# Kernel tuning notes

Hardware: AMD Instinct MI355X
Metric: run time of the kernel (lower is better)

Reference implementation:

```python
import jax, jax.numpy as jnp
import numpy as np

B, DIM, HEADS, WS, H, W = 8, 192, 6, 8, 128, 128
HD = DIM // HEADS


def _make_coords(h, w, ws):
    # matches torch buffers: channel 0 = x (width axis), channel 1 = y (height axis)
    ref_w = jnp.linspace(-1.0, 1.0, w)
    ref_h = jnp.linspace(-1.0, 1.0, h)
    img_ref = jnp.stack(jnp.meshgrid(ref_w, ref_h, indexing='ij'), 0).transpose(0, 2, 1)  # (2,h,w)
    wh, ww = h // ws, w // ws
    win_ref = img_ref.reshape(2, wh, ws, ww, ws).mean(axis=(2, 4)).reshape(2, wh, 1, ww, 1)
    bch = jnp.arange(ws) * 2.0 / (h - 1); bch = bch - bch.mean()
    bcw = jnp.arange(ws) * 2.0 / (w - 1); bcw = bcw - bcw.mean()
    ech = jnp.tile(bch, wh)                      # (wh*ws,)
    ecw = jnp.tile(bcw, ww)                      # (ww*ws,)
    offs = jnp.stack(jnp.meshgrid(ecw, ech, indexing='ij'), 0).transpose(0, 2, 1)  # (2, wh*ws, ww*ws)
    offs = offs.reshape(2, wh, ws, ww, ws)
    return win_ref + offs, offs


def _rel_index(ws):
    ch, cw = np.meshgrid(np.arange(ws), np.arange(ws), indexing='ij')
    cf = np.stack([ch.ravel(), cw.ravel()])           # (2, ws*ws)
    rel = cf[:, :, None] - cf[:, None, :]             # (2, n, n)
    return jnp.asarray((rel[0] + ws - 1) * (2 * ws - 1) + (rel[1] + ws - 1))


def _grid_sample(img, grid):
    # F.grid_sample: bilinear, padding_mode='zeros', align_corners=True
    # img (N,C,H,W), grid (N,Ho,Wo,2) with [..,0]=x, [..,1]=y in [-1,1]
    n, c, h, w = img.shape
    gx = (grid[..., 0] + 1.0) * 0.5 * (w - 1)
    gy = (grid[..., 1] + 1.0) * 0.5 * (h - 1)
    x0 = jnp.floor(gx); y0 = jnp.floor(gy)
    wx1 = gx - x0; wy1 = gy - y0

    def gather(ix, iy, wgt):
        valid = (ix >= 0) & (ix <= w - 1) & (iy >= 0) & (iy <= h - 1)
        ixc = jnp.clip(ix, 0, w - 1).astype(jnp.int32)
        iyc = jnp.clip(iy, 0, h - 1).astype(jnp.int32)
        vals = jax.vmap(lambda im, yy, xx: im[:, yy, xx])(img, iyc, ixc)  # (N,C,Ho,Wo)
        return vals * (wgt * valid)[:, None]

    return (gather(x0, y0, (1 - wx1) * (1 - wy1)) + gather(x0 + 1, y0, wx1 * (1 - wy1))
            + gather(x0, y0 + 1, (1 - wx1) * wy1) + gather(x0 + 1, y0 + 1, wx1 * wy1))


def _forward(x, var, qkv_w, qkv_b, bias_w, bias_b, scale_w, scale_b, proj_w, proj_b, rel_table):
    b, c, h, w = x.shape
    wh, ww = h // WS, w // WS
    n_pred = b * HEADS
    base, offs = _make_coords(h, w, WS)

    topk = int(0.8 * h * w)
    var3 = var.reshape(b, c, h * w)
    _, idx = jax.lax.top_k(var3, topk)
    bi = jnp.arange(b)[:, None, None]; ci = jnp.arange(c)[None, :, None]
    mask = jnp.zeros((b, c, h * w), bool).at[bi, ci, idx].set(True)
    x_var = x * jnp.where(mask, 1.0, 0.6).reshape(b, c, h, w).astype(x.dtype)

    # sampling biases/scales: AvgPool(ws) -> LeakyReLU -> 1x1 conv
    pooled = jax.nn.leaky_relu(x_var.reshape(b, c, wh, WS, ww, WS).mean(axis=(3, 5)))
    biases = (jnp.einsum('bchw,oc->bohw', pooled, bias_w) + bias_b[None, :, None, None])
    biases = biases.reshape(n_pred, 2, wh, ww) / jnp.array([w // WS, h // WS], x.dtype)[None, :, None, None]
    scales = (jnp.einsum('bchw,oc->bohw', pooled, scale_w) + scale_b[None, :, None, None]).reshape(n_pred, 2, wh, ww)

    coords = base[None] + offs[None] * scales[:, :, :, None, :, None] + biases[:, :, :, None, :, None]
    grid = coords.transpose(0, 2, 3, 4, 5, 1).reshape(n_pred, h, w, 2)

    # qkv 1x1 conv, split into per-head maps
    qkv = jnp.einsum('bchw,oc->bohw', x, qkv_w) + qkv_b[None, :, None, None]
    qkv = qkv.reshape(b, 3, HEADS, HD, h, w).transpose(1, 0, 2, 3, 4, 5).reshape(3, n_pred, HD, h, w)
    q, k, v = qkv[0], qkv[1], qkv[2]

    ks = _grid_sample(k, grid)
    vs = _grid_sample(v, grid)

    def to_windows(t):  # (b*heads, hd, h, w) -> (b*wh*ww, heads, ws*ws, hd)
        return t.reshape(b, HEADS, HD, wh, WS, ww, WS).transpose(0, 3, 5, 1, 4, 6, 2).reshape(b * wh * ww, HEADS, WS * WS, HD)

    qw, kw, vw = to_windows(q), to_windows(ks), to_windows(vs)
    scores = jnp.einsum('wnid,wnjd->wnij', qw, kw) * (HD ** -0.5)
    rel_bias = rel_table[_rel_index(WS)].transpose(2, 0, 1)  # (heads, ws*ws, ws*ws)
    attn = jax.nn.softmax(scores + rel_bias[None], axis=-1)
    out = jnp.einsum('wnij,wnjd->wnid', attn, vw)
    out = out.reshape(b, wh, ww, HEADS, WS, WS, HD).transpose(0, 3, 6, 1, 4, 2, 5).reshape(b, c, h, w)
    return jnp.einsum('bchw,oc->bohw', out, proj_w) + proj_b[None, :, None, None]


def setup_inputs() -> dict:
    key = jax.random.key(0)
    ks = jax.random.split(key, 8)
    f = jnp.float32
    return {
        'x': jax.random.normal(ks[0], (B, DIM, H, W), f),
        'var': jax.random.uniform(ks[1], (B, DIM, H, W), f),
        'qkv_w': jax.random.normal(ks[2], (3 * DIM, DIM), f) * 0.05,
        'qkv_b': jnp.zeros((3 * DIM,), f),
        'bias_w': jax.random.normal(ks[3], (2 * HEADS, DIM), f) * 0.05,
        'bias_b': jnp.zeros((2 * HEADS,), f),
        'scale_w': jax.random.normal(ks[4], (2 * HEADS, DIM), f) * 0.05,
        'scale_b': jnp.zeros((2 * HEADS,), f),
        'proj_w': jax.random.normal(ks[5], (DIM, DIM), f) * 0.05,
        'proj_b': jnp.zeros((DIM,), f),
        'rel_table': jax.random.normal(ks[6], ((2 * WS - 1) ** 2, HEADS), f) * 0.02,
    }


def reference(x, var, qkv_w, qkv_b, bias_w, bias_b, scale_w, scale_b, proj_w, proj_b, rel_table):
    return _forward(x, var, qkv_w, qkv_b, bias_w, bias_b, scale_w, scale_b, proj_w, proj_b, rel_table)
```

## Files before the change

kernel.cpp:

```cpp
#include <hip/hip_runtime.h>
#include <hip/hip_bf16.h>
#include <math.h>

constexpr int BB = 8, CCH = 192, IH = 128, IW = 128;
constexpr int WSZ = 8;
constexpr int NWIN = 256;
constexpr int NH = 6, HDIM = 32;
constexpr int NPIX = IH * IW;
constexpr int TOPK = 13107;

typedef __attribute__((ext_vector_type(8))) short bf16x8;
typedef __attribute__((ext_vector_type(4))) float f32x4;
typedef __attribute__((ext_vector_type(4))) unsigned short u16x4;
typedef __attribute__((ext_vector_type(8))) unsigned short u16x8;

__device__ __forceinline__ unsigned short f2bf(float f) {
    __hip_bfloat16 h = __float2bfloat16(f);
    return __builtin_bit_cast(unsigned short, h);
}
__device__ __forceinline__ float bf2f(unsigned short u) {
    return __uint_as_float((unsigned)u << 16);
}
__device__ __forceinline__ unsigned monot(float f) {
    unsigned u = __float_as_uint(f);
    return (u & 0x80000000u) ? ~u : (u | 0x80000000u);
}

__global__ __launch_bounds__(512) void k1_pool(const float* __restrict__ x,
                                               const float* __restrict__ var,
                                               float* __restrict__ pooled) {
    int row = blockIdx.x;
    const float4* vrow4 = (const float4*)(var + (size_t)row * NPIX);
    const float4* xrow4 = (const float4*)(x + (size_t)row * NPIX);
    const float* xrow = x + (size_t)row * NPIX;
    int tid = threadIdx.x;
    int wv = tid >> 6, lane = tid & 63;

    constexpr int CAP = 320;
    __shared__ unsigned histP[2][2048];
    __shared__ unsigned hist256[256];
    __shared__ unsigned wtot[8];
    __shared__ unsigned s_prefix, s_rem, s_cnt, s_thr, s_need;
    __shared__ unsigned candKey[CAP], candIdx[CAP];
    __shared__ unsigned cand_cnt, eq_cnt;
    __shared__ unsigned eq_idx[64];
    __shared__ float pooled_s[256];

    for (int i = tid; i < 2 * 2048; i += 512) ((unsigned*)histP)[i] = 0;
    if (tid < 256) pooled_s[tid] = 0.f;
    if (tid == 0) { cand_cnt = 0; eq_cnt = 0; }
    __syncthreads();

    int hc = lane & 1;
#pragma unroll
    for (int j = 0; j < 8; ++j) {
        float4 v4 = vrow4[tid + 512 * j];
        float vv[4] = {v4.x, v4.y, v4.z, v4.w};
#pragma unroll
        for (int c = 0; c < 4; ++c) {
            unsigned bk = monot(vv[c]) >> 20;
            atomicAdd(&histP[hc][bk >> 1], 1u << ((bk & 1) << 4));
        }
    }
    __syncthreads();

    {
        unsigned h8[8]; unsigned tsum = 0;
#pragma unroll
        for (int w = 0; w < 4; ++w) {
            unsigned w0 = histP[0][tid * 4 + w];
            unsigned w1 = histP[1][tid * 4 + w];
            h8[2 * w]     = (w0 & 0xFFFFu) + (w1 & 0xFFFFu);
            h8[2 * w + 1] = (w0 >> 16) + (w1 >> 16);
            tsum += h8[2 * w] + h8[2 * w + 1];
        }
        unsigned s = tsum;
#pragma unroll
        for (int off = 1; off < 64; off <<= 1) {
            unsigned t = __shfl(s, lane + off);
            if (lane + off < 64) s += t;
        }
        if (lane == 0) wtot[wv] = s;
        __syncthreads();
        unsigned crossTot = 0;
        for (int w = wv + 1; w < 8; ++w) crossTot += wtot[w];
        unsigned above = crossTot + (s - tsum);
        if (above < TOPK && above + tsum >= TOPK) {
            unsigned cum = above;
            for (int i = 7; i >= 0; --i) {
                if (cum < TOPK && cum + h8[i] >= TOPK) {
                    s_prefix = (unsigned)(tid * 8 + i);
                    s_rem = TOPK - cum;
                    s_cnt = h8[i];
                }
                cum += h8[i];
            }
        }
    }
    __syncthreads();

    unsigned prefix = s_prefix, rem2 = s_rem, cnt = s_cnt;
    int prefbits = 12;

    while (cnt > CAP && prefbits < 32) {
        int nb = (32 - prefbits >= 8) ? 8 : (32 - prefbits);
        int nbuck = 1 << nb;
        __syncthreads();
        for (int i = tid; i < nbuck; i += 512) hist256[i] = 0;
        __syncthreads();
        int shift = 32 - prefbits - nb;
#pragma unroll
        for (int j = 0; j < 8; ++j) {
            float4 v4 = vrow4[tid + 512 * j];
            float vv[4] = {v4.x, v4.y, v4.z, v4.w};
#pragma unroll
            for (int c = 0; c < 4; ++c) {
                unsigned mm = monot(vv[c]);
                if ((mm >> (nb + shift)) == prefix)
                    atomicAdd(&hist256[(mm >> shift) & (nbuck - 1)], 1u);
            }
        }
        __syncthreads();
        if (wv == 0) {
            int bpl = nbuck > 64 ? nbuck / 64 : 1;
            int nlanes = nbuck / bpl;
            unsigned hh[4] = {0, 0, 0, 0};
            unsigned lsum = 0;
#pragma unroll
            for (int i = 0; i < 4; ++i) {
                if (i < bpl && lane < nlanes) hh[i] = hist256[lane * bpl + i];
                lsum += hh[i];
            }
            unsigned s = lsum;
#pragma unroll
            for (int off = 1; off < 64; off <<= 1) {
                unsigned t = __shfl(s, lane + off);
                if (lane + off < 64) s += t;
            }
            unsigned above = s - lsum;
            if (lane < nlanes && above < rem2 && above + lsum >= rem2) {
                unsigned cum = above;
                for (int i = bpl - 1; i >= 0; --i) {
                    if (cum < rem2 && cum + hh[i] >= rem2) {
                        s_prefix = (prefix << nb) | (unsigned)(lane * bpl + i);
                        s_rem = rem2 - cum;
                        s_cnt = hh[i];
                    }
                    cum += hh[i];
                }
            }
        }
        __syncthreads();
        prefix = s_prefix; rem2 = s_rem; cnt = s_cnt;
        prefbits += nb;
    }

    int pshift = 32 - prefbits;

#pragma unroll
    for (int j = 0; j < 8; ++j) {
        float4 v4 = vrow4[tid + 512 * j];
        float4 x4 = xrow4[tid + 512 * j];
        float vv[4] = {v4.x, v4.y, v4.z, v4.w};
        float xv[4] = {x4.x, x4.y, x4.z, x4.w};
        float part = 0.f;
#pragma unroll
        for (int c = 0; c < 4; ++c) {
            unsigned mm = monot(vv[c]);
            unsigned g = (pshift == 0) ? mm : (mm >> pshift);
            float mult = (g > prefix) ? 1.0f : 0.6f;
            if (g == prefix) {
                unsigned pos = atomicAdd(&cand_cnt, 1u);
                if (pos < CAP) {
                    candKey[pos] = mm;
                    candIdx[pos] = (unsigned)(4 * tid + 2048 * j + c);
                }
            }
            part += xv[c] * mult;
        }
        part += __shfl_xor(part, 1);
        part += __shfl_xor(part, 32);
        if ((lane & 1) == 0 && lane < 32)
            atomicAdd(&pooled_s[(2 * j + (tid >> 8)) * 16 + ((tid >> 1) & 15)], part);
    }
    __syncthreads();

    int cc = (int)min(cand_cnt, (unsigned)CAP);
    for (int ci = tid; ci < cc; ci += 512) {
        unsigned my = candKey[ci];
        unsigned kgt = 0, keq = 0;
        for (int e = 0; e < cc; ++e) {
            unsigned o = candKey[e];
            kgt += (o > my);
            keq += (o == my);
        }
        if (kgt < rem2 && kgt + keq >= rem2) {
            s_thr = my;
            s_need = rem2 - kgt;
        }
    }
    __syncthreads();
    unsigned thr = s_thr, need_eq = s_need;
    for (int ci = tid; ci < cc; ci += 512)
        if (candKey[ci] == thr) {
            unsigned pos = atomicAdd(&eq_cnt, 1u);
            if (pos < 64) eq_idx[pos] = candIdx[ci];
        }
    __syncthreads();
    int ecnt = (int)min(eq_cnt, 64u);
    if (tid == 0) {
        for (int a = 1; a < ecnt; ++a) {
            unsigned key = eq_idx[a]; int q = a - 1;
            while (q >= 0 && eq_idx[q] > key) { eq_idx[q + 1] = eq_idx[q]; --q; }
            eq_idx[q + 1] = key;
        }
    }
    __syncthreads();

    for (int ci = tid; ci < cc; ci += 512) {
        unsigned key = candKey[ci], idx = candIdx[ci];
        bool inset;
        if (key > thr) inset = true;
        else if (key < thr) inset = false;
        else {
            unsigned rank = 0;
            for (int e = 0; e < ecnt; ++e) rank += (eq_idx[e] < idx);
            inset = (rank < need_eq);
        }
        if (inset) {
            int y = (int)(idx >> 7), xx = (int)(idx & 127);
            atomicAdd(&pooled_s[(y >> 3) * 16 + (xx >> 3)], 0.4f * xrow[idx]);
        }
    }
    __syncthreads();

    if (tid < 256) {
        float s = pooled_s[tid] * (1.0f / 64.0f);
        float pv = s > 0.f ? s : 0.01f * s;
        pooled[(size_t)row * NWIN + tid] = pv;
    }
}

__global__ __launch_bounds__(64) void k2_sb(const float* __restrict__ pooled,
                                            const float* __restrict__ bias_w,
                                            const float* __restrict__ bias_b,
                                            const float* __restrict__ scale_w,
                                            const float* __restrict__ scale_b,
                                            float* __restrict__ sb) {
    int blk = blockIdx.x;
    int b = blk / NWIN, w = blk % NWIN;
    int tid = threadIdx.x;
    __shared__ float pcol[CCH];
    __shared__ float res[24];
    for (int c = tid; c < CCH; c += 64) pcol[c] = pooled[(size_t)(b * CCH + c) * NWIN + w];
    __syncthreads();
    if (tid < 24) {
        bool isScale = tid >= 12;
        int o = isScale ? tid - 12 : tid;
        const float* Wt = isScale ? scale_w : bias_w;
        float acc = 0.f;
        for (int c = 0; c < CCH; ++c) acc += Wt[o * CCH + c] * pcol[c];
        acc += (isScale ? scale_b[o] : bias_b[o]);
        if (!isScale) acc *= (1.0f / 16.0f);
        res[tid] = acc;
    }
    __syncthreads();
    if (tid < NH) {
        int p = b * NH + tid;
        float4 v;
        v.x = res[12 + 2 * tid];
        v.y = res[12 + 2 * tid + 1];
        v.z = res[2 * tid];
        v.w = res[2 * tid + 1];
        ((float4*)sb)[(size_t)p * NWIN + w] = v;
    }
}

__global__ __launch_bounds__(256) void kw_conv(const float* __restrict__ qkv_w,
                                               const float* __restrict__ proj_w,
                                               unsigned short* __restrict__ wbf) {
    int i4 = blockIdx.x * 256 + threadIdx.x;
    float4 v = (i4 < 27648) ? ((const float4*)qkv_w)[i4]
                            : ((const float4*)proj_w)[i4 - 27648];
    u16x4 pk = { f2bf(v.x), f2bf(v.y), f2bf(v.z), f2bf(v.w) };
    ((u16x4*)wbf)[i4] = pk;
}

__global__ __launch_bounds__(256) void k0_xpose(const float* __restrict__ x,
                                                unsigned short* __restrict__ xt) {
    __shared__ unsigned short T[64][200];
    int px0 = blockIdx.x * 64;
    int b = blockIdx.y;
    int tid = threadIdx.x;
    int px = tid & 63, cg = tid >> 6;

#pragma unroll
    for (int j8 = 0; j8 < 6; ++j8) {
        u16x8 pk;
#pragma unroll
        for (int j = 0; j < 8; ++j)
            pk[j] = f2bf(x[(size_t)(b * CCH + cg * 48 + j8 * 8 + j) * NPIX + px0 + px]);
        *(u16x8*)&T[px][cg * 48 + j8 * 8] = pk;
    }
    __syncthreads();
#pragma unroll
    for (int i = 0; i < 6; ++i) {
        int u = tid + 256 * i;
        int p2 = u / 24, cb = u % 24;
        *(u16x8*)&xt[((size_t)(b * NPIX) + px0 + p2) * CCH + cb * 8] = *(const u16x8*)&T[p2][cb * 8];
    }
}

template <bool FAST>
__global__ __launch_bounds__(256) void k3_mfma(const float* __restrict__ x,
                                               const unsigned short* __restrict__ xt,
                                               const unsigned short* __restrict__ wq,
                                               const float* __restrict__ qkv_b,
                                               unsigned short* __restrict__ qb,
                                               unsigned short* __restrict__ kb,
                                               unsigned short* __restrict__ vb) {
    constexpr int BN = 128, KC = 64, KCP = 72;
    __shared__ unsigned short Ws[CCH][KCP];
    __shared__ unsigned short Xt[BN][KCP];
    int px0 = blockIdx.x * BN;
    int t = blockIdx.y, b = blockIdx.z;
    int o0 = t * CCH;
    int tid = threadIdx.x;
    int wv = tid >> 6, lane = tid & 63, lr = lane & 15, lg = lane >> 4;

    f32x4 acc[3][8];
#pragma unroll
    for (int i = 0; i < 3; ++i)
#pragma unroll
        for (int j = 0; j < 8; ++j) acc[i][j] = (f32x4){0.f, 0.f, 0.f, 0.f};

    int spx = tid & 127, skg = tid >> 7;

    for (int k0 = 0; k0 < CCH; k0 += KC) {
#pragma unroll
        for (int i = 0; i < 6; ++i) {
            int u = tid + 256 * i;
            int o = u >> 3, kb8 = u & 7;
            *(u16x8*)&Ws[o][kb8 * 8] = *(const u16x8*)&wq[(size_t)(o0 + o) * CCH + k0 + kb8 * 8];
        }
        if (FAST) {
#pragma unroll
            for (int i = 0; i < 4; ++i) {
                int u = tid + 256 * i;
                int px = u >> 3, kb8 = u & 7;
                *(u16x8*)&Xt[px][kb8 * 8] =
                    *(const u16x8*)&xt[((size_t)(b * NPIX) + px0 + px) * CCH + k0 + kb8 * 8];
            }
        } else {
            const float* xcol = &x[(size_t)(b * CCH + k0 + skg * 32) * NPIX + px0 + spx];
#pragma unroll
            for (int j8 = 0; j8 < 4; ++j8) {
                u16x8 pk;
#pragma unroll
                for (int j = 0; j < 8; ++j) pk[j] = f2bf(xcol[(size_t)(j8 * 8 + j) * NPIX]);
                *(u16x8*)&Xt[spx][skg * 32 + j8 * 8] = pk;
            }
        }
        __syncthreads();
#pragma unroll
        for (int kk = 0; kk < KC; kk += 32) {
            bf16x8 af[3], bfr[8];
#pragma unroll
            for (int i = 0; i < 3; ++i)
                af[i] = *(const bf16x8*)&Ws[wv * 48 + i * 16 + lr][kk + lg * 8];
#pragma unroll
            for (int j = 0; j < 8; ++j)
                bfr[j] = *(const bf16x8*)&Xt[j * 16 + lr][kk + lg * 8];
#pragma unroll
            for (int i = 0; i < 3; ++i)
#pragma unroll
                for (int j = 0; j < 8; ++j)
                    acc[i][j] = __builtin_amdgcn_mfma_f32_16x16x32_bf16(af[i], bfr[j], acc[i][j], 0, 0, 0);
        }
        __syncthreads();
    }

#pragma unroll
    for (int i = 0; i < 3; ++i) {
        int och = wv * 48 + i * 16 + lg * 4;
        float b0 = qkv_b[o0 + och], b1 = qkv_b[o0 + och + 1];
        float b2 = qkv_b[o0 + och + 2], b3 = qkv_b[o0 + och + 3];
#pragma unroll
        for (int j = 0; j < 8; ++j) {
            int px = px0 + lr + j * 16;
            u16x4 pk = { f2bf(acc[i][j][0] + b0), f2bf(acc[i][j][1] + b1),
                         f2bf(acc[i][j][2] + b2), f2bf(acc[i][j][3] + b3) };
            if (t == 0) {
                *(u16x4*)&qb[((size_t)b * NPIX + px) * CCH + och] = pk;
            } else {
                int head = och >> 5, d = och & 31;
                unsigned short* dst = (t == 1) ? kb : vb;
                *(u16x4*)&dst[(((size_t)(b * NH + head)) * NPIX + px) * HDIM + d] = pk;
            }
        }
    }
}

__global__ __launch_bounds__(256) void k4_attn(unsigned short* __restrict__ qatt,
                                               const unsigned short* __restrict__ kb,
                                               const unsigned short* __restrict__ vb,
                                               const float* __restrict__ sb,
                                               const float* __restrict__ rel_table) {
    int tid = threadIdx.x;
    int wv = tid >> 6, lane = tid & 63, lr = lane & 15, lg = lane >> 4;
    int head = blockIdx.y, b = blockIdx.z;
    int win = blockIdx.x * 4 + wv;
    int wy = win >> 4, wx = win & 15;
    int p = b * NH + head;

    __shared__ float rel_s[225];
    __shared__ unsigned short Vl[4][64][33];
    __shared__ unsigned short Pl[4][64][68];

    if (tid < 225) rel_s[tid] = rel_table[tid * NH + head];

    bf16x8 qf[4];
#pragma unroll
    for (int tq = 0; tq < 4; ++tq) {
        int q = tq * 16 + lr;
        int pix = (wy * 8 + (q >> 3)) * IW + wx * 8 + (q & 7);
        qf[tq] = *(const bf16x8*)&qatt[((size_t)b * NPIX + pix) * CCH + head * HDIM + lg * 8];
    }

    float4 sbv = ((const float4*)sb)[(size_t)p * NWIN + win];
    bf16x8 kf[4];
#pragma unroll
    for (int mi = 0; mi < 4; ++mi) {
        int px = mi * 16 + lr;
        int dy = px >> 3, dx = px & 7;
        int yg = wy * 8 + dy, xg = wx * 8 + dx;
        float gx = -1.0f + xg * (2.0f / 127.0f) + ((float)dx - 3.5f) * (2.0f / 127.0f) * sbv.x + sbv.z;
        float gy = -1.0f + yg * (2.0f / 127.0f) + ((float)dy - 3.5f) * (2.0f / 127.0f) * sbv.y + sbv.w;
        float fx = (gx + 1.0f) * 0.5f * 127.0f;
        float fy = (gy + 1.0f) * 0.5f * 127.0f;
        float x0f = floorf(fx), y0f = floorf(fy);
        float wx1 = fx - x0f, wy1 = fy - y0f;
        int ix0 = (int)x0f, iy0 = (int)y0f;
        int ix1 = ix0 + 1, iy1 = iy0 + 1;
        float w00 = (1.0f - wx1) * (1.0f - wy1);
        float w10 = wx1 * (1.0f - wy1);
        float w01 = (1.0f - wx1) * wy1;
        float w11 = wx1 * wy1;
        bool vX0 = (ix0 >= 0) && (ix0 < IW), vX1 = (ix1 >= 0) && (ix1 < IW);
        bool vY0 = (iy0 >= 0) && (iy0 < IH), vY1 = (iy1 >= 0) && (iy1 < IH);
        if (!(vX0 && vY0)) w00 = 0.f;
        if (!(vX1 && vY0)) w10 = 0.f;
        if (!(vX0 && vY1)) w01 = 0.f;
        if (!(vX1 && vY1)) w11 = 0.f;
        int cx0 = min(max(ix0, 0), IW - 1), cx1 = min(max(ix1, 0), IW - 1);
        int cy0 = min(max(iy0, 0), IH - 1), cy1 = min(max(iy1, 0), IH - 1);
        size_t r00 = ((size_t)p * NPIX + cy0 * IW + cx0) * HDIM + lg * 8;
        size_t r10 = ((size_t)p * NPIX + cy0 * IW + cx1) * HDIM + lg * 8;
        size_t r01 = ((size_t)p * NPIX + cy1 * IW + cx0) * HDIM + lg * 8;
        size_t r11 = ((size_t)p * NPIX + cy1 * IW + cx1) * HDIM + lg * 8;
        u16x8 k00 = *(const u16x8*)&kb[r00], k10 = *(const u16x8*)&kb[r10];
        u16x8 k01 = *(const u16x8*)&kb[r01], k11 = *(const u16x8*)&kb[r11];
        u16x8 v00 = *(const u16x8*)&vb[r00], v10 = *(const u16x8*)&vb[r10];
        u16x8 v01 = *(const u16x8*)&vb[r01], v11 = *(const u16x8*)&vb[r11];
#pragma unroll
        for (int c = 0; c < 8; ++c) {
            float kvv = w00 * bf2f(k00[c]) + w10 * bf2f(k10[c]) +
                        w01 * bf2f(k01[c]) + w11 * bf2f(k11[c]);
            float vvv = w00 * bf2f(v00[c]) + w10 * bf2f(v10[c]) +
                        w01 * bf2f(v01[c]) + w11 * bf2f(v11[c]);
            kf[mi][c] = (short)f2bf(kvv);
            Vl[wv][px][lg * 8 + c] = f2bf(vvv);
        }
    }

    f32x4 acc[4][4];
#pragma unroll
    for (int tk = 0; tk < 4; ++tk)
#pragma unroll
        for (int tq = 0; tq < 4; ++tq) acc[tk][tq] = (f32x4){0.f, 0.f, 0.f, 0.f};
#pragma unroll
    for (int tk = 0; tk < 4; ++tk)
#pragma unroll
        for (int tq = 0; tq < 4; ++tq)
            acc[tk][tq] = __builtin_amdgcn_mfma_f32_16x16x32_bf16(kf[tk], qf[tq], acc[tk][tq], 0, 0, 0);

    __syncthreads();

    const float scale = 0.17677669529663688f;
    int qh[4], qwv[4];
#pragma unroll
    for (int tq = 0; tq < 4; ++tq) { int q = tq * 16 + lr; qh[tq] = q >> 3; qwv[tq] = q & 7; }
    float mx[4] = {-1e30f, -1e30f, -1e30f, -1e30f};
#pragma unroll
    for (int tk = 0; tk < 4; ++tk)
#pragma unroll
        for (int r = 0; r < 4; ++r) {
            int key = tk * 16 + lg * 4 + r;
            int kh = key >> 3, kw = key & 7;
#pragma unroll
            for (int tq = 0; tq < 4; ++tq) {
                float v = acc[tk][tq][r] * scale + rel_s[(qh[tq] - kh + 7) * 15 + (qwv[tq] - kw + 7)];
                acc[tk][tq][r] = v;
                mx[tq] = fmaxf(mx[tq], v);
            }
        }
#pragma unroll
    for (int tq = 0; tq < 4; ++tq) {
        mx[tq] = fmaxf(mx[tq], __shfl_xor(mx[tq], 16));
        mx[tq] = fmaxf(mx[tq], __shfl_xor(mx[tq], 32));
    }
    float sm[4] = {0.f, 0.f, 0.f, 0.f};
#pragma unroll
    for (int tk = 0; tk < 4; ++tk)
#pragma unroll
        for (int tq = 0; tq < 4; ++tq)
#pragma unroll
            for (int r = 0; r < 4; ++r) {
                float e = __expf(acc[tk][tq][r] - mx[tq]);
                acc[tk][tq][r] = e;
                sm[tq] += e;
            }
    float inv[4];
#pragma unroll
    for (int tq = 0; tq < 4; ++tq) {
        float s = sm[tq];
        s += __shfl_xor(s, 16);
        s += __shfl_xor(s, 32);
        inv[tq] = 1.0f / s;
    }
#pragma unroll
    for (int tq = 0; tq < 4; ++tq)
#pragma unroll
        for (int tk = 0; tk < 4; ++tk) {
            u16x4 pk = { f2bf(acc[tk][tq][0] * inv[tq]), f2bf(acc[tk][tq][1] * inv[tq]),
                         f2bf(acc[tk][tq][2] * inv[tq]), f2bf(acc[tk][tq][3] * inv[tq]) };
            *(u16x4*)&Pl[wv][tq * 16 + lr][tk * 16 + lg * 4] = pk;
        }

    __syncthreads();

    f32x4 o[4][2];
#pragma unroll
    for (int mq = 0; mq < 4; ++mq)
#pragma unroll
        for (int nd = 0; nd < 2; ++nd) o[mq][nd] = (f32x4){0.f, 0.f, 0.f, 0.f};
#pragma unroll
    for (int ks = 0; ks < 2; ++ks) {
        bf16x8 Af[4];
#pragma unroll
        for (int mq = 0; mq < 4; ++mq) {
            u16x4 lo = *(const u16x4*)&Pl[wv][mq * 16 + lr][ks * 32 + lg * 8];
            u16x4 hi = *(const u16x4*)&Pl[wv][mq * 16 + lr][ks * 32 + lg * 8 + 4];
#pragma unroll
            for (int c = 0; c < 4; ++c) { Af[mq][c] = (short)lo[c]; Af[mq][c + 4] = (short)hi[c]; }
        }
        bf16x8 Bf[2];
#pragma unroll
        for (int nd = 0; nd < 2; ++nd)
#pragma unroll
            for (int j = 0; j < 8; ++j)
                Bf[nd][j] = (short)Vl[wv][ks * 32 + lg * 8 + j][nd * 16 + lr];
#pragma unroll
        for (int mq = 0; mq < 4; ++mq)
#pragma unroll
            for (int nd = 0; nd < 2; ++nd)
                o[mq][nd] = __builtin_amdgcn_mfma_f32_16x16x32_bf16(Af[mq], Bf[nd], o[mq][nd], 0, 0, 0);
    }

#pragma unroll
    for (int mq = 0; mq < 4; ++mq)
#pragma unroll
        for (int nd = 0; nd < 2; ++nd)
#pragma unroll
            for (int r = 0; r < 4; ++r) {
                int q = mq * 16 + lg * 4 + r;
                int pix = (wy * 8 + (q >> 3)) * IW + wx * 8 + (q & 7);
                qatt[((size_t)b * NPIX + pix) * CCH + head * HDIM + nd * 16 + lr] = f2bf(o[mq][nd][r]);
            }
}

__global__ __launch_bounds__(256) void k5_mfma(const unsigned short* __restrict__ att,
                                               const unsigned short* __restrict__ wp,
                                               const float* __restrict__ proj_b,
                                               float* __restrict__ out) {
    constexpr int BN = 128, KC = 64, KCP = 72;
    __shared__ unsigned short Ws[CCH][KCP];
    __shared__ unsigned short Xt[BN][KCP];
    int px0 = blockIdx.x * BN;
    int b = blockIdx.y;
    int tid = threadIdx.x;
    int wv = tid >> 6, lane = tid & 63, lr = lane & 15, lg = lane >> 4;

    f32x4 acc[3][8];
#pragma unroll
    for (int i = 0; i < 3; ++i)
#pragma unroll
        for (int j = 0; j < 8; ++j) acc[i][j] = (f32x4){0.f, 0.f, 0.f, 0.f};

    int spx = tid & 127, skg = tid >> 7;

    for (int k0 = 0; k0 < CCH; k0 += KC) {
#pragma unroll
        for (int i = 0; i < 6; ++i) {
            int u = tid + 256 * i;
            int o = u >> 3, kb8 = u & 7;
            *(u16x8*)&Ws[o][kb8 * 8] = *(const u16x8*)&wp[(size_t)o * CCH + k0 + kb8 * 8];
        }
        {
            const unsigned short* arow = &att[((size_t)b * NPIX + px0 + spx) * CCH + k0 + skg * 32];
#pragma unroll
            for (int j8 = 0; j8 < 4; ++j8)
                *(u16x8*)&Xt[spx][skg * 32 + j8 * 8] = *(const u16x8*)&arow[j8 * 8];
        }
        __syncthreads();
#pragma unroll
        for (int kk = 0; kk < KC; kk += 32) {
            bf16x8 af[3], bfr[8];
#pragma unroll
            for (int i = 0; i < 3; ++i)
                af[i] = *(const bf16x8*)&Ws[wv * 48 + i * 16 + lr][kk + lg * 8];
#pragma unroll
            for (int j = 0; j < 8; ++j)
                bfr[j] = *(const bf16x8*)&Xt[j * 16 + lr][kk + lg * 8];
#pragma unroll
            for (int i = 0; i < 3; ++i)
#pragma unroll
                for (int j = 0; j < 8; ++j)
                    acc[i][j] = __builtin_amdgcn_mfma_f32_16x16x32_bf16(af[i], bfr[j], acc[i][j], 0, 0, 0);
        }
        __syncthreads();
    }

#pragma unroll
    for (int i = 0; i < 3; ++i) {
        int och = wv * 48 + i * 16 + lg * 4;
#pragma unroll
        for (int r = 0; r < 4; ++r) {
            float bias = proj_b[och + r];
            size_t base = (size_t)(b * CCH + och + r) * NPIX + px0 + lr;
#pragma unroll
            for (int j = 0; j < 8; ++j)
                out[base + j * 16] = acc[i][j][r] + bias;
        }
    }
}

extern "C" void kernel_launch(void* const* d_in, const int* in_sizes, int n_in,
                              void* d_out, int out_size, void* d_ws, size_t ws_size,
                              hipStream_t stream) {
    const float* x = (const float*)d_in[0];
    const float* var = (const float*)d_in[1];
    const float* qkv_w = (const float*)d_in[2];
    const float* qkv_b = (const float*)d_in[3];
    const float* bias_w = (const float*)d_in[4];
    const float* bias_b = (const float*)d_in[5];
    const float* scale_w = (const float*)d_in[6];
    const float* scale_b = (const float*)d_in[7];
    const float* proj_w = (const float*)d_in[8];
    const float* proj_b = (const float*)d_in[9];
    const float* rel_table = (const float*)d_in[10];
    float* out = (float*)d_out;

    char* ws = (char*)d_ws;
    float* pooled = (float*)ws;
    float* sb = (float*)(ws + 1572864ull);
    unsigned short* wbf = (unsigned short*)ws;
    unsigned short* wq_bf = wbf;
    unsigned short* wp_bf = wbf + 110592;
    const size_t elemQ = (size_t)BB * CCH * NPIX;
    unsigned short* q = (unsigned short*)(ws + 1769472ull);
    unsigned short* k = q + elemQ;
    unsigned short* v = k + elemQ;
    unsigned short* xt = v + elemQ;

    size_t need_base = 1769472ull + 3ull * elemQ * 2;
    size_t need_fast = 1769472ull + 4ull * elemQ * 2;
    if (ws_size < need_base) return;
    bool fast = ws_size >= need_fast;

    k1_pool<<<dim3(BB * CCH), dim3(512), 0, stream>>>(x, var, pooled);
    k2_sb<<<dim3(BB * NWIN), dim3(64), 0, stream>>>(pooled, bias_w, bias_b, scale_w, scale_b, sb);
    kw_conv<<<dim3(144), dim3(256), 0, stream>>>(qkv_w, proj_w, wbf);
    if (fast) {
        k0_xpose<<<dim3(NPIX / 64, BB), dim3(256), 0, stream>>>(x, xt);
        k3_mfma<true><<<dim3(NPIX / 128, 3, BB), dim3(256), 0, stream>>>(x, xt, wq_bf, qkv_b, q, k, v);
    } else {
        k3_mfma<false><<<dim3(NPIX / 128, 3, BB), dim3(256), 0, stream>>>(x, xt, wq_bf, qkv_b, q, k, v);
    }
    k4_attn<<<dim3(NWIN / 4, NH, BB), dim3(256), 0, stream>>>(q, k, v, sb, rel_table);
    k5_mfma<<<dim3(NPIX / 128, BB), dim3(256), 0, stream>>>(q, wp_bf, proj_b, out);
}
```

Measured before the change: 288.1 us.

## Merge pooling, transpose, weight conversion and projections into fewer interleaved launches

Combines the top-k pooling and the x transpose into one launch with interleaved block roles, and merges the scale/bias projection with the QKV GEMM into a second launch. The separate weight-to-bf16 conversion kernel is removed; the GEMMs now convert fp32 weights on the fly while filling shared memory. This cuts the launch count from seven to four and lets independent work overlap. In exchange, each GEMM block redoes the fp32-to-bf16 conversion and reads twice as many weight bytes, and the mixed-role blocks share one LDS allocation sized for the larger role, which may limit occupancy.

```diff
diff --git a/kernel.cpp b/kernel.cpp
--- a/kernel.cpp
+++ b/kernel.cpp
@@ -26,29 +26,72 @@
     return (u & 0x80000000u) ? ~u : (u | 0x80000000u);
 }
 
-__global__ __launch_bounds__(512) void k1_pool(const float* __restrict__ x,
-                                               const float* __restrict__ var,
-                                               float* __restrict__ pooled) {
-    int row = blockIdx.x;
+struct K1Smem {
+    unsigned histP[2][2048];
+    unsigned hist256[256];
+    unsigned wtot[8];
+    unsigned s_prefix, s_rem, s_cnt, s_thr, s_need;
+    unsigned candKey[320], candIdx[320];
+    unsigned cand_cnt, eq_cnt;
+    unsigned eq_idx[64];
+    float pooled_s[256];
+};
+struct K0Smem {
+    unsigned short T[64][200];
+};
+constexpr size_t MEGA1_SMEM = sizeof(K0Smem) > sizeof(K1Smem) ? sizeof(K0Smem) : sizeof(K1Smem);
+
+__global__ __launch_bounds__(512) void mega1(const float* __restrict__ x,
+                                             const float* __restrict__ var,
+                                             float* __restrict__ pooled,
+                                             unsigned short* __restrict__ xt,
+                                             int fast) {
+    __shared__ __align__(16) char smem[MEGA1_SMEM];
+    int id = blockIdx.x;
+    int tid = threadIdx.x;
+    int wv = tid >> 6, lane = tid & 63;
+
+    int role, sub;
+    if (fast) {
+        int g = id / 7, r = id % 7;
+        if (r < 3) { role = 0; sub = 3 * g + r; }
+        else       { role = 1; sub = 4 * g + (r - 3); }
+    } else {
+        role = 0; sub = id;
+    }
+
+    if (role == 1) {
+        K0Smem& S0 = *(K0Smem*)smem;
+        int b = sub >> 8, px0 = (sub & 255) * 64;
+        int px = tid & 63, cg = tid >> 6;
+#pragma unroll
+        for (int j8 = 0; j8 < 3; ++j8) {
+            u16x8 pk;
+#pragma unroll
+            for (int j = 0; j < 8; ++j)
+                pk[j] = f2bf(x[(size_t)(b * CCH + cg * 24 + j8 * 8 + j) * NPIX + px0 + px]);
+            *(u16x8*)&S0.T[px][cg * 24 + j8 * 8] = pk;
+        }
+        __syncthreads();
+#pragma unroll
+        for (int i = 0; i < 3; ++i) {
+            int u = tid + 512 * i;
+            int p2 = u / 24, cb = u % 24;
+            *(u16x8*)&xt[((size_t)(b * NPIX) + px0 + p2) * CCH + cb * 8] = *(const u16x8*)&S0.T[p2][cb * 8];
+        }
+        return;
+    }
+
+    K1Smem& S = *(K1Smem*)smem;
+    int row = sub;
     const float4* vrow4 = (const float4*)(var + (size_t)row * NPIX);
     const float4* xrow4 = (const float4*)(x + (size_t)row * NPIX);
     const float* xrow = x + (size_t)row * NPIX;
-    int tid = threadIdx.x;
-    int wv = tid >> 6, lane = tid & 63;
-
     constexpr int CAP = 320;
-    __shared__ unsigned histP[2][2048];
-    __shared__ unsigned hist256[256];
-    __shared__ unsigned wtot[8];
-    __shared__ unsigned s_prefix, s_rem, s_cnt, s_thr, s_need;
-    __shared__ unsigned candKey[CAP], candIdx[CAP];
-    __shared__ unsigned cand_cnt, eq_cnt;
-    __shared__ unsigned eq_idx[64];
-    __shared__ float pooled_s[256];
-
-    for (int i = tid; i < 2 * 2048; i += 512) ((unsigned*)histP)[i] = 0;
-    if (tid < 256) pooled_s[tid] = 0.f;
-    if (tid == 0) { cand_cnt = 0; eq_cnt = 0; }
+
+    for (int i = tid; i < 2 * 2048; i += 512) ((unsigned*)S.histP)[i] = 0;
+    if (tid < 256) S.pooled_s[tid] = 0.f;
+    if (tid == 0) { S.cand_cnt = 0; S.eq_cnt = 0; }
     __syncthreads();
 
     int hc = lane & 1;
@@ -59,7 +102,7 @@
 #pragma unroll
         for (int c = 0; c < 4; ++c) {
             unsigned bk = monot(vv[c]) >> 20;
-            atomicAdd(&histP[hc][bk >> 1], 1u << ((bk & 1) << 4));
+            atomicAdd(&S.histP[hc][bk >> 1], 1u << ((bk & 1) << 4));
         }
     }
     __syncthreads();
@@ -68,8 +111,8 @@
         unsigned h8[8]; unsigned tsum = 0;
 #pragma unroll
         for (int w = 0; w < 4; ++w) {
-            unsigned w0 = histP[0][tid * 4 + w];
-            unsigned w1 = histP[1][tid * 4 + w];
+            unsigned w0 = S.histP[0][tid * 4 + w];
+            unsigned w1 = S.histP[1][tid * 4 + w];
             h8[2 * w]     = (w0 & 0xFFFFu) + (w1 & 0xFFFFu);
             h8[2 * w + 1] = (w0 >> 16) + (w1 >> 16);
             tsum += h8[2 * w] + h8[2 * w + 1];
@@ -80,18 +123,18 @@
             unsigned t = __shfl(s, lane + off);
             if (lane + off < 64) s += t;
         }
-        if (lane == 0) wtot[wv] = s;
+        if (lane == 0) S.wtot[wv] = s;
         __syncthreads();
         unsigned crossTot = 0;
-        for (int w = wv + 1; w < 8; ++w) crossTot += wtot[w];
+        for (int w = wv + 1; w < 8; ++w) crossTot += S.wtot[w];
         unsigned above = crossTot + (s - tsum);
         if (above < TOPK && above + tsum >= TOPK) {
             unsigned cum = above;
             for (int i = 7; i >= 0; --i) {
                 if (cum < TOPK && cum + h8[i] >= TOPK) {
-                    s_prefix = (unsigned)(tid * 8 + i);
-                    s_rem = TOPK - cum;
-                    s_cnt = h8[i];
+                    S.s_prefix = (unsigned)(tid * 8 + i);
+                    S.s_rem = TOPK - cum;
+                    S.s_cnt = h8[i];
                 }
                 cum += h8[i];
             }
@@ -99,14 +142,14 @@
     }
     __syncthreads();
 
-    unsigned prefix = s_prefix, rem2 = s_rem, cnt = s_cnt;
+    unsigned prefix = S.s_prefix, rem2 = S.s_rem, cnt = S.s_cnt;
     int prefbits = 12;
 
     while (cnt > CAP && prefbits < 32) {
         int nb = (32 - prefbits >= 8) ? 8 : (32 - prefbits);
         int nbuck = 1 << nb;
         __syncthreads();
-        for (int i = tid; i < nbuck; i += 512) hist256[i] = 0;
+        for (int i = tid; i < nbuck; i += 512) S.hist256[i] = 0;
         __syncthreads();
         int shift = 32 - prefbits - nb;
 #pragma unroll
@@ -117,7 +160,7 @@
             for (int c = 0; c < 4; ++c) {
                 unsigned mm = monot(vv[c]);
                 if ((mm >> (nb + shift)) == prefix)
-                    atomicAdd(&hist256[(mm >> shift) & (nbuck - 1)], 1u);
+                    atomicAdd(&S.hist256[(mm >> shift) & (nbuck - 1)], 1u);
             }
         }
         __syncthreads();
@@ -128,7 +171,7 @@
             unsigned lsum = 0;
 #pragma unroll
             for (int i = 0; i < 4; ++i) {
-                if (i < bpl && lane < nlanes) hh[i] = hist256[lane * bpl + i];
+                if (i < bpl && lane < nlanes) hh[i] = S.hist256[lane * bpl + i];
                 lsum += hh[i];
             }
             unsigned s = lsum;
@@ -142,16 +185,16 @@
                 unsigned cum = above;
                 for (int i = bpl - 1; i >= 0; --i) {
                     if (cum < rem2 && cum + hh[i] >= rem2) {
-                        s_prefix = (prefix << nb) | (unsigned)(lane * bpl + i);
-                        s_rem = rem2 - cum;
-                        s_cnt = hh[i];
+                        S.s_prefix = (prefix << nb) | (unsigned)(lane * bpl + i);
+                        S.s_rem = rem2 - cum;
+                        S.s_cnt = hh[i];
                     }
                     cum += hh[i];
                 }
             }
         }
         __syncthreads();
-        prefix = s_prefix; rem2 = s_rem; cnt = s_cnt;
+        prefix = S.s_prefix; rem2 = S.s_rem; cnt = S.s_cnt;
         prefbits += nb;
     }
 
@@ -170,10 +213,10 @@
             unsigned g = (pshift == 0) ? mm : (mm >> pshift);
             float mult = (g > prefix) ? 1.0f : 0.6f;
             if (g == prefix) {
-                unsigned pos = atomicAdd(&cand_cnt, 1u);
+                unsigned pos = atomicAdd(&S.cand_cnt, 1u);
                 if (pos < CAP) {
-                    candKey[pos] = mm;
-                    candIdx[pos] = (unsigned)(4 * tid + 2048 * j + c);
+                    S.candKey[pos] = mm;
+                    S.candIdx[pos] = (unsigned)(4 * tid + 2048 * j + c);
                 }
             }
             part += xv[c] * mult;
@@ -181,151 +224,123 @@
         part += __shfl_xor(part, 1);
         part += __shfl_xor(part, 32);
         if ((lane & 1) == 0 && lane < 32)
-            atomicAdd(&pooled_s[(2 * j + (tid >> 8)) * 16 + ((tid >> 1) & 15)], part);
-    }
-    __syncthreads();
-
-    int cc = (int)min(cand_cnt, (unsigned)CAP);
+            atomicAdd(&S.pooled_s[(2 * j + (tid >> 8)) * 16 + ((tid >> 1) & 15)], part);
+    }
+    __syncthreads();
+
+    int cc = (int)min(S.cand_cnt, (unsigned)CAP);
     for (int ci = tid; ci < cc; ci += 512) {
-        unsigned my = candKey[ci];
+        unsigned my = S.candKey[ci];
         unsigned kgt = 0, keq = 0;
         for (int e = 0; e < cc; ++e) {
-            unsigned o = candKey[e];
+            unsigned o = S.candKey[e];
             kgt += (o > my);
             keq += (o == my);
         }
         if (kgt < rem2 && kgt + keq >= rem2) {
-            s_thr = my;
-            s_need = rem2 - kgt;
-        }
-    }
-    __syncthreads();
-    unsigned thr = s_thr, need_eq = s_need;
+            S.s_thr = my;
+            S.s_need = rem2 - kgt;
+        }
+    }
+    __syncthreads();
+    unsigned thr = S.s_thr, need_eq = S.s_need;
     for (int ci = tid; ci < cc; ci += 512)
-        if (candKey[ci] == thr) {
-            unsigned pos = atomicAdd(&eq_cnt, 1u);
-            if (pos < 64) eq_idx[pos] = candIdx[ci];
-        }
-    __syncthreads();
-    int ecnt = (int)min(eq_cnt, 64u);
+        if (S.candKey[ci] == thr) {
+            unsigned pos = atomicAdd(&S.eq_cnt, 1u);
+            if (pos < 64) S.eq_idx[pos] = S.candIdx[ci];
+        }
+    __syncthreads();
+    int ecnt = (int)min(S.eq_cnt, 64u);
     if (tid == 0) {
         for (int a = 1; a < ecnt; ++a) {
-            unsigned key = eq_idx[a]; int q = a - 1;
-            while (q >= 0 && eq_idx[q] > key) { eq_idx[q + 1] = eq_idx[q]; --q; }
-            eq_idx[q + 1] = key;
+            unsigned key = S.eq_idx[a]; int q = a - 1;
+            while (q >= 0 && S.eq_idx[q] > key) { S.eq_idx[q + 1] = S.eq_idx[q]; --q; }
+            S.eq_idx[q + 1] = key;
         }
     }
     __syncthreads();
 
     for (int ci = tid; ci < cc; ci += 512) {
-        unsigned key = candKey[ci], idx = candIdx[ci];
+        unsigned key = S.candKey[ci], idx = S.candIdx[ci];
         bool inset;
         if (key > thr) inset = true;
         else if (key < thr) inset = false;
         else {
             unsigned rank = 0;
-            for (int e = 0; e < ecnt; ++e) rank += (eq_idx[e] < idx);
+            for (int e = 0; e < ecnt; ++e) rank += (S.eq_idx[e] < idx);
             inset = (rank < need_eq);
         }
         if (inset) {
             int y = (int)(idx >> 7), xx = (int)(idx & 127);
-            atomicAdd(&pooled_s[(y >> 3) * 16 + (xx >> 3)], 0.4f * xrow[idx]);
+            atomicAdd(&S.pooled_s[(y >> 3) * 16 + (xx >> 3)], 0.4f * xrow[idx]);
         }
     }
     __syncthreads();
 
     if (tid < 256) {
-        float s = pooled_s[tid] * (1.0f / 64.0f);
+        float s = S.pooled_s[tid] * (1.0f / 64.0f);
         float pv = s > 0.f ? s : 0.01f * s;
         pooled[(size_t)row * NWIN + tid] = pv;
     }
 }
 
-__global__ __launch_bounds__(64) void k2_sb(const float* __restrict__ pooled,
-                                            const float* __restrict__ bias_w,
-                                            const float* __restrict__ bias_b,
-                                            const float* __restrict__ scale_w,
-                                            const float* __restrict__ scale_b,
-                                            float* __restrict__ sb) {
-    int blk = blockIdx.x;
-    int b = blk / NWIN, w = blk % NWIN;
-    int tid = threadIdx.x;
-    __shared__ float pcol[CCH];
-    __shared__ float res[24];
-    for (int c = tid; c < CCH; c += 64) pcol[c] = pooled[(size_t)(b * CCH + c) * NWIN + w];
-    __syncthreads();
-    if (tid < 24) {
-        bool isScale = tid >= 12;
-        int o = isScale ? tid - 12 : tid;
-        const float* Wt = isScale ? scale_w : bias_w;
-        float acc = 0.f;
-        for (int c = 0; c < CCH; ++c) acc += Wt[o * CCH + c] * pcol[c];
-        acc += (isScale ? scale_b[o] : bias_b[o]);
-        if (!isScale) acc *= (1.0f / 16.0f);
-        res[tid] = acc;
-    }
-    __syncthreads();
-    if (tid < NH) {
-        int p = b * NH + tid;
-        float4 v;
-        v.x = res[12 + 2 * tid];
-        v.y = res[12 + 2 * tid + 1];
-        v.z = res[2 * tid];
-        v.w = res[2 * tid + 1];
-        ((float4*)sb)[(size_t)p * NWIN + w] = v;
-    }
-}
-
-__global__ __launch_bounds__(256) void kw_conv(const float* __restrict__ qkv_w,
-                                               const float* __restrict__ proj_w,
-                                               unsigned short* __restrict__ wbf) {
-    int i4 = blockIdx.x * 256 + threadIdx.x;
-    float4 v = (i4 < 27648) ? ((const float4*)qkv_w)[i4]
-                            : ((const float4*)proj_w)[i4 - 27648];
-    u16x4 pk = { f2bf(v.x), f2bf(v.y), f2bf(v.z), f2bf(v.w) };
-    ((u16x4*)wbf)[i4] = pk;
-}
-
-__global__ __launch_bounds__(256) void k0_xpose(const float* __restrict__ x,
-                                                unsigned short* __restrict__ xt) {
-    __shared__ unsigned short T[64][200];
-    int px0 = blockIdx.x * 64;
-    int b = blockIdx.y;
-    int tid = threadIdx.x;
-    int px = tid & 63, cg = tid >> 6;
-
-#pragma unroll
-    for (int j8 = 0; j8 < 6; ++j8) {
-        u16x8 pk;
-#pragma unroll
-        for (int j = 0; j < 8; ++j)
-            pk[j] = f2bf(x[(size_t)(b * CCH + cg * 48 + j8 * 8 + j) * NPIX + px0 + px]);
-        *(u16x8*)&T[px][cg * 48 + j8 * 8] = pk;
-    }
-    __syncthreads();
-#pragma unroll
-    for (int i = 0; i < 6; ++i) {
-        int u = tid + 256 * i;
-        int p2 = u / 24, cb = u % 24;
-        *(u16x8*)&xt[((size_t)(b * NPIX) + px0 + p2) * CCH + cb * 8] = *(const u16x8*)&T[p2][cb * 8];
-    }
-}
-
 template <bool FAST>
-__global__ __launch_bounds__(256) void k3_mfma(const float* __restrict__ x,
-                                               const unsigned short* __restrict__ xt,
-                                               const unsigned short* __restrict__ wq,
-                                               const float* __restrict__ qkv_b,
-                                               unsigned short* __restrict__ qb,
-                                               unsigned short* __restrict__ kb,
-                                               unsigned short* __restrict__ vb) {
+__global__ __launch_bounds__(256) void mega2(const float* __restrict__ x,
+                                             const unsigned short* __restrict__ xt,
+                                             const float* __restrict__ qkv_w,
+                                             const float* __restrict__ qkv_b,
+                                             unsigned short* __restrict__ qb,
+                                             unsigned short* __restrict__ kb,
+                                             unsigned short* __restrict__ vb,
+                                             const float* __restrict__ pooled,
+                                             const float* __restrict__ bias_w,
+                                             const float* __restrict__ bias_b,
+                                             const float* __restrict__ scale_w,
+                                             const float* __restrict__ scale_b,
+                                             float* __restrict__ sb) {
     constexpr int BN = 128, KC = 64, KCP = 72;
     __shared__ unsigned short Ws[CCH][KCP];
     __shared__ unsigned short Xt[BN][KCP];
-    int px0 = blockIdx.x * BN;
-    int t = blockIdx.y, b = blockIdx.z;
+    int id = blockIdx.x;
+    int tid = threadIdx.x;
+    int g = id / 7, r = id % 7;
+
+    if (r == 0) {
+        float* pcol = (float*)&Ws[0][0];
+        float* res = pcol + 4 * CCH;
+        int wv = tid >> 6, lane = tid & 63;
+        int blk = g * 4 + wv;
+        int b = blk >> 8, w = blk & 255;
+        for (int c = lane; c < CCH; c += 64) pcol[wv * CCH + c] = pooled[(size_t)(b * CCH + c) * NWIN + w];
+        __syncthreads();
+        if (lane < 24) {
+            bool isScale = lane >= 12;
+            int o = isScale ? lane - 12 : lane;
+            const float* Wt = isScale ? scale_w : bias_w;
+            float acc = 0.f;
+            for (int c = 0; c < CCH; ++c) acc += Wt[o * CCH + c] * pcol[wv * CCH + c];
+            acc += (isScale ? scale_b[o] : bias_b[o]);
+            if (!isScale) acc *= (1.0f / 16.0f);
+            res[wv * 24 + lane] = acc;
+        }
+        __syncthreads();
+        if (lane < NH) {
+            int p = b * NH + lane;
+            float4 v;
+            v.x = res[wv * 24 + 12 + 2 * lane];
+            v.y = res[wv * 24 + 12 + 2 * lane + 1];
+            v.z = res[wv * 24 + 2 * lane];
+            v.w = res[wv * 24 + 2 * lane + 1];
+            ((float4*)sb)[(size_t)p * NWIN + w] = v;
+        }
+        return;
+    }
+
+    int k3id = 6 * g + (r - 1);
+    int px0 = (k3id & 127) * BN;
+    int t = (k3id >> 7) % 3;
+    int b = k3id / 384;
     int o0 = t * CCH;
-    int tid = threadIdx.x;
     int wv = tid >> 6, lane = tid & 63, lr = lane & 15, lg = lane >> 4;
 
     f32x4 acc[3][8];
@@ -337,11 +352,11 @@
     int spx = tid & 127, skg = tid >> 7;
 
     for (int k0 = 0; k0 < CCH; k0 += KC) {
-#pragma unroll
-        for (int i = 0; i < 6; ++i) {
-            int u = tid + 256 * i;
-            int o = u >> 3, kb8 = u & 7;
-            *(u16x8*)&Ws[o][kb8 * 8] = *(const u16x8*)&wq[(size_t)(o0 + o) * CCH + k0 + kb8 * 8];
+        for (int idx4 = tid; idx4 < CCH * KC / 4; idx4 += 256) {
+            int o = idx4 >> 4, k4i = (idx4 & 15) * 4;
+            float4 w4 = *(const float4*)&qkv_w[(size_t)(o0 + o) * CCH + k0 + k4i];
+            u16x4 pk = { f2bf(w4.x), f2bf(w4.y), f2bf(w4.z), f2bf(w4.w) };
+            *(u16x4*)&Ws[o][k4i] = pk;
         }
         if (FAST) {
 #pragma unroll
@@ -580,7 +595,7 @@
 }
 
 __global__ __launch_bounds__(256) void k5_mfma(const unsigned short* __restrict__ att,
-                                               const unsigned short* __restrict__ wp,
+                                               const float* __restrict__ proj_w,
                                                const float* __restrict__ proj_b,
                                                float* __restrict__ out) {
     constexpr int BN = 128, KC = 64, KCP = 72;
@@ -600,11 +615,11 @@
     int spx = tid & 127, skg = tid >> 7;
 
     for (int k0 = 0; k0 < CCH; k0 += KC) {
-#pragma unroll
-        for (int i = 0; i < 6; ++i) {
-            int u = tid + 256 * i;
-            int o = u >> 3, kb8 = u & 7;
-            *(u16x8*)&Ws[o][kb8 * 8] = *(const u16x8*)&wp[(size_t)o * CCH + k0 + kb8 * 8];
+        for (int idx4 = tid; idx4 < CCH * KC / 4; idx4 += 256) {
+            int o = idx4 >> 4, k4i = (idx4 & 15) * 4;
+            float4 w4 = *(const float4*)&proj_w[(size_t)o * CCH + k0 + k4i];
+            u16x4 pk = { f2bf(w4.x), f2bf(w4.y), f2bf(w4.z), f2bf(w4.w) };
+            *(u16x4*)&Ws[o][k4i] = pk;
         }
         {
             const unsigned short* arow = &att[((size_t)b * NPIX + px0 + spx) * CCH + k0 + skg * 32];
@@ -664,9 +679,6 @@
     char* ws = (char*)d_ws;
     float* pooled = (float*)ws;
     float* sb = (float*)(ws + 1572864ull);
-    unsigned short* wbf = (unsigned short*)ws;
-    unsigned short* wq_bf = wbf;
-    unsigned short* wp_bf = wbf + 110592;
     const size_t elemQ = (size_t)BB * CCH * NPIX;
     unsigned short* q = (unsigned short*)(ws + 1769472ull);
     unsigned short* k = q + elemQ;
@@ -678,15 +690,16 @@
     if (ws_size < need_base) return;
     bool fast = ws_size >= need_fast;
 
-    k1_pool<<<dim3(BB * CCH), dim3(512), 0, stream>>>(x, var, pooled);
-    k2_sb<<<dim3(BB * NWIN), dim3(64), 0, stream>>>(pooled, bias_w, bias_b, scale_w, scale_b, sb);
-    kw_conv<<<dim3(144), dim3(256), 0, stream>>>(qkv_w, proj_w, wbf);
+    mega1<<<dim3(fast ? 3584 : 1536), dim3(512), 0, stream>>>(x, var, pooled, xt, fast ? 1 : 0);
+
     if (fast) {
-        k0_xpose<<<dim3(NPIX / 64, BB), dim3(256), 0, stream>>>(x, xt);
-        k3_mfma<true><<<dim3(NPIX / 128, 3, BB), dim3(256), 0, stream>>>(x, xt, wq_bf, qkv_b, q, k, v);
+        mega2<true><<<dim3(3584), dim3(256), 0, stream>>>(x, xt, qkv_w, qkv_b, q, k, v,
+                                                          pooled, bias_w, bias_b, scale_w, scale_b, sb);
     } else {
-        k3_mfma<false><<<dim3(NPIX / 128, 3, BB), dim3(256), 0, stream>>>(x, xt, wq_bf, qkv_b, q, k, v);
-    }
+        mega2<false><<<dim3(3584), dim3(256), 0, stream>>>(x, xt, qkv_w, qkv_b, q, k, v,
+                                                           pooled, bias_w, bias_b, scale_w, scale_b, sb);
+    }
+
     k4_attn<<<dim3(NWIN / 4, NH, BB), dim3(256), 0, stream>>>(q, k, v, sb, rel_table);
-    k5_mfma<<<dim3(NPIX / 128, BB), dim3(256), 0, stream>>>(q, wp_bf, proj_b, out);
+    k5_mfma<<<dim3(NPIX / 128, BB), dim3(256), 0, stream>>>(q, proj_w, proj_b, out);
 }
```

After: 346.7 us. +20.3%, slower.
